# Kernel tuning notes

Hardware: AMD Instinct MI355X
Metric: run time of the kernel (lower is better)

The kernel has to match this reference:

```python
import jax, jax.numpy as jnp
import numpy as np

B, T, D, H = 8192, 2048, 2, 2


def setup_inputs() -> dict:
    key = jax.random.key(0)
    ks = jax.random.split(key, 7)
    return {
        "x": jax.random.normal(ks[0], (B, T, D), dtype=jnp.float32),
        "h0": jax.random.normal(ks[1], (B, H), dtype=jnp.float32),
        "c0": jax.random.normal(ks[2], (B, H), dtype=jnp.float32),
        "w_ih": jax.random.normal(ks[3], (4 * H, D), dtype=jnp.float32),
        "w_hh": jax.random.normal(ks[4], (4 * H, H), dtype=jnp.float32),
        "b_ih": jax.random.normal(ks[5], (4 * H,), dtype=jnp.float32),
        "b_hh": jax.random.normal(ks[6], (4 * H,), dtype=jnp.float32),
    }


def reference(x, h0, c0, w_ih, w_hh, b_ih, b_hh):
    # Precompute input projections for all timesteps in one GEMM: (T, B, 4H)
    xg = jnp.einsum("btd,gd->tbg", x, w_ih) + b_ih

    def step(carry, xt_g):
        h, c = carry
        gates = xt_g + h @ w_hh.T + b_hh  # (B, 4H)
        i, f, g, o = jnp.split(gates, 4, axis=-1)  # torch lstm_cell gate order: i,f,g,o
        c = jax.nn.sigmoid(f) * c + jax.nn.sigmoid(i) * jnp.tanh(g)
        h = jax.nn.sigmoid(o) * jnp.tanh(c)
        return (h, c), None

    (h, c), _ = jax.lax.scan(step, (h0, c0), xg)
    return c
```

## Files before the change

### kernel.cpp

```cpp
#include <hip/hip_runtime.h>


#define LOG2E 1.4426950408889634f

template <int CTRL>
__device__ __forceinline__ float qdpp(float v) {
    int i = __builtin_bit_cast(int, v);
    i = __builtin_amdgcn_update_dpp(0, i, CTRL, 0xf, 0xf, true);
    return __builtin_bit_cast(float, i);
}
#define DPP_HSEL        0x14
#define DPP_BCAST2      0xAA
#define DPP_BCAST3      0xFF
#define DPP_SWAP2       0x4E
#define DPP_HALF_MIRROR 0x141

__global__ __launch_bounds__(64, 1) void lstm_oct_kernel(
    const float* __restrict__ x,
    const float* __restrict__ h0,
    const float* __restrict__ c0,
    const float* __restrict__ w_ih,
    const float* __restrict__ w_hh,
    const float* __restrict__ b_ih,
    const float* __restrict__ b_hh,
    float* __restrict__ out,
    int B, int T)
{
    const int tid = blockIdx.x * blockDim.x + threadIdx.x;
    const int e = tid >> 3;
    const int q = tid & 7;
    if (e >= B) return;

    const int r = (q < 4) ? q : 11 - q;
    const bool isTanh = (q >= 6);
    const bool inQ1   = (q >= 4);
    const bool sel45  = (q == 4) || (q == 5);
    const bool selMid = (q >= 2) && (q <= 5);

    const float a = isTanh ? (2.0f * LOG2E) : (-LOG2E);
    const float m = isTanh ? (-4.0f * LOG2E) : 1.0f;
    const float d = isTanh ? (2.0f * LOG2E) : 0.0f;

    const float wi0 = w_ih[2 * r] * a, wi1 = w_ih[2 * r + 1] * a;
    const float wh0 = w_hh[2 * r] * a, wh1 = w_hh[2 * r + 1] * a;
    const float bias = (b_ih[r] + b_hh[r]) * a;

    const int col = (q & 1) ^ ((q >> 2) & 1);
    float h = h0[2 * e + col];
    float c = c0[2 * e + col] * (2.0f * LOG2E);

    const int NI = T >> 1;
    const float4* __restrict__ xp =
        reinterpret_cast<const float4*>(x) + (size_t)e * NI;

    auto step = [&](float x0, float x1) {
        float hm  = qdpp<DPP_HSEL>(h);
        float hs  = inQ1 ? hm : h;
        float hh0 = qdpp<DPP_BCAST2>(hs);
        float hh1 = qdpp<DPP_BCAST3>(hs);
        float ax = fmaf(wi1, x1, fmaf(wi0, x0, bias));
        float g  = fmaf(wh1, hh1, fmaf(wh0, hh0, ax));
        float n  = fmaf(m, __builtin_amdgcn_rcpf(1.0f + __builtin_amdgcn_exp2f(g)), d);
        float mv = qdpp<DPP_HALF_MIRROR>(n);
        float X = sel45  ? mv : n;
        float Y = selMid ? c  : mv;
        float p = X * Y;
        float ps = qdpp<DPP_SWAP2>(p);
        c = p + ps;
        float tc = fmaf(-2.0f, __builtin_amdgcn_rcpf(1.0f + __builtin_amdgcn_exp2f(c)), 1.0f);
        float Z = sel45 ? n : mv;
        h = Z * tc;
    };

    constexpr int BV = 8;
    float4 A[BV], Bb[BV];

    auto loadbuf = [&](float4* buf, int batch) {
#pragma unroll
        for (int j = 0; j < BV; ++j) buf[j] = xp[batch * BV + j];
    };
    auto consume = [&](const float4* buf) {
#pragma unroll
        for (int j = 0; j < BV; ++j) {
            step(buf[j].x, buf[j].y);
            step(buf[j].z, buf[j].w);
        }
    };

    const int nb = NI / BV;
    int bi = 0;
    if (nb >= 2) {
        loadbuf(A, 0);
        loadbuf(Bb, 1);
        for (bi = 0; bi + 1 < nb; bi += 2) {
            consume(A);
            if (bi + 2 < nb) loadbuf(A, bi + 2);
            consume(Bb);
            if (bi + 3 < nb) loadbuf(Bb, bi + 3);
        }
        if (bi < nb) { consume(A); ++bi; }
    }
    for (int i = bi * BV; i < NI; ++i) {
        float4 v = xp[i];
        step(v.x, v.y);
        step(v.z, v.w);
    }

    if (q < 2) out[2 * e + q] = c * (0.5f / LOG2E);
}

extern "C" void kernel_launch(void* const* d_in, const int* in_sizes, int n_in,
                              void* d_out, int out_size, void* d_ws, size_t ws_size,
                              hipStream_t stream) {
    const float* x    = (const float*)d_in[0];
    const float* h0   = (const float*)d_in[1];
    const float* c0   = (const float*)d_in[2];
    const float* w_ih = (const float*)d_in[3];
    const float* w_hh = (const float*)d_in[4];
    const float* b_ih = (const float*)d_in[5];
    const float* b_hh = (const float*)d_in[6];
    float* out = (float*)d_out;

    const int B = in_sizes[1] / 2;
    const int T = in_sizes[0] / (B * 2);

    const int threads = B * 8;
    dim3 block(64);
    dim3 grid((threads + 63) / 64);
    hipLaunchKernelGGL(lstm_oct_kernel, grid, block, 0, stream,
                       x, h0, c0, w_ih, w_hh, b_ih, b_hh, out, B, T);
}
```

Measured before the change: 323.7 us.

## Fold output gate into recurrent weights and compute tanh(c) from exp products

Restructures the recurrent step so h is never formed explicitly. Each lane keeps tanh(c) and folds the sigmoid(o) factor into per-step effective recurrent weights, taken from neighbouring lanes through masked DPP moves, so the h broadcast and its select drop off the critical dependency chain. tanh(c) is computed from the product of exp2 of the two partial products, letting that exp2 start before the swap-add finishes. In exchange it adds extra DPP moves and multiplies per step, and exp2 of the separate terms can overflow where exp2 of their sum would not, which changes numerics at extreme values.

```diff
diff --git a/kernel.cpp b/kernel.cpp
--- a/kernel.cpp
+++ b/kernel.cpp
@@ -6,16 +6,25 @@
 template <int CTRL>
 __device__ __forceinline__ float qdpp(float v) {
     int i = __builtin_bit_cast(int, v);
-    i = __builtin_amdgcn_update_dpp(0, i, CTRL, 0xf, 0xf, true);
+    i = __builtin_amdgcn_update_dpp(0, i, CTRL, 0xF, 0xF, true);
     return __builtin_bit_cast(float, i);
 }
-#define DPP_HSEL        0x14
-#define DPP_BCAST2      0xAA
-#define DPP_BCAST3      0xFF
-#define DPP_SWAP2       0x4E
-#define DPP_HALF_MIRROR 0x141
+template <int CTRL, int BANK>
+__device__ __forceinline__ float mdpp(float old, float v) {
+    int i = __builtin_amdgcn_update_dpp(__builtin_bit_cast(int, old),
+                                        __builtin_bit_cast(int, v),
+                                        CTRL, 0xF, BANK, false);
+    return __builtin_bit_cast(float, i);
+}
+#define DPP_MIRROR8 0x141
+#define DPP_SWAP2   0x4E
+#define DPP_COLSWP  0xB1
+#define DPP_ZB_OWN0 0xEE
+#define DPP_ZB_OWN1 0x44
+#define DPP_ZB_OTH0 0xBB
+#define DPP_ZB_OTH1 0x11
 
-__global__ __launch_bounds__(64, 1) void lstm_oct_kernel(
+__global__ __launch_bounds__(64, 1) void lstm_oct_nh_kernel(
     const float* __restrict__ x,
     const float* __restrict__ h0,
     const float* __restrict__ c0,
@@ -33,43 +42,50 @@
 
     const int r = (q < 4) ? q : 11 - q;
     const bool isTanh = (q >= 6);
-    const bool inQ1   = (q >= 4);
     const bool sel45  = (q == 4) || (q == 5);
     const bool selMid = (q >= 2) && (q <= 5);
+    const int col = (q & 1) ^ ((q >> 2) & 1);
 
     const float a = isTanh ? (2.0f * LOG2E) : (-LOG2E);
     const float m = isTanh ? (-4.0f * LOG2E) : 1.0f;
     const float d = isTanh ? (2.0f * LOG2E) : 0.0f;
 
-    const float wi0 = w_ih[2 * r] * a, wi1 = w_ih[2 * r + 1] * a;
-    const float wh0 = w_hh[2 * r] * a, wh1 = w_hh[2 * r + 1] * a;
+    const float wx0 = w_ih[2 * r] * a, wx1 = w_ih[2 * r + 1] * a;
     const float bias = (b_ih[r] + b_hh[r]) * a;
+    const float AwhOwn = w_hh[2 * r + col] * a;
+    const float AwhOth = w_hh[2 * r + (1 - col)] * a;
 
-    const int col = (q & 1) ^ ((q >> 2) & 1);
-    float h = h0[2 * e + col];
-    float c = c0[2 * e + col] * (2.0f * LOG2E);
+    float tc = h0[2 * e + col];
+    float cs = c0[2 * e + col] * (2.0f * LOG2E);
+    float WOwn = AwhOwn;
+    float WOth = AwhOth;
 
     const int NI = T >> 1;
     const float4* __restrict__ xp =
         reinterpret_cast<const float4*>(x) + (size_t)e * NI;
 
     auto step = [&](float x0, float x1) {
-        float hm  = qdpp<DPP_HSEL>(h);
-        float hs  = inQ1 ? hm : h;
-        float hh0 = qdpp<DPP_BCAST2>(hs);
-        float hh1 = qdpp<DPP_BCAST3>(hs);
-        float ax = fmaf(wi1, x1, fmaf(wi0, x0, bias));
-        float g  = fmaf(wh1, hh1, fmaf(wh0, hh0, ax));
-        float n  = fmaf(m, __builtin_amdgcn_rcpf(1.0f + __builtin_amdgcn_exp2f(g)), d);
-        float mv = qdpp<DPP_HALF_MIRROR>(n);
-        float X = sel45  ? mv : n;
-        float Y = selMid ? c  : mv;
+        float tco = qdpp<DPP_COLSWP>(tc);
+        float ax  = fmaf(wx1, x1, fmaf(wx0, x0, bias));
+        float g   = fmaf(WOth, tco, fmaf(WOwn, tc, ax));
+        float n   = fmaf(m, __builtin_amdgcn_rcpf(1.0f + __builtin_amdgcn_exp2f(g)), d);
+        float mv  = qdpp<DPP_MIRROR8>(n);
+        float X = sel45 ? mv : n;
+        float Y = selMid ? cs : mv;
         float p = X * Y;
         float ps = qdpp<DPP_SWAP2>(p);
-        c = p + ps;
-        float tc = fmaf(-2.0f, __builtin_amdgcn_rcpf(1.0f + __builtin_amdgcn_exp2f(c)), 1.0f);
+        cs = p + ps;
+        float Ep  = __builtin_amdgcn_exp2f(p);
+        float Eps = qdpp<DPP_SWAP2>(Ep);
+        float r2  = __builtin_amdgcn_rcpf(fmaf(Ep, Eps, 1.0f));
+        tc = fmaf(-2.0f, r2, 1.0f);
         float Z = sel45 ? n : mv;
-        h = Z * tc;
+        float zbOwn = mdpp<DPP_ZB_OWN0, 0x5>(Z, Z);
+        zbOwn = mdpp<DPP_ZB_OWN1, 0xA>(zbOwn, Z);
+        float zbOth = mdpp<DPP_ZB_OTH0, 0x5>(Z, Z);
+        zbOth = mdpp<DPP_ZB_OTH1, 0xA>(zbOth, Z);
+        WOwn = AwhOwn * zbOwn;
+        WOth = AwhOth * zbOth;
     };
 
     constexpr int BV = 8;
@@ -106,7 +122,7 @@
         step(v.z, v.w);
     }
 
-    if (q < 2) out[2 * e + q] = c * (0.5f / LOG2E);
+    if (q < 2) out[2 * e + q] = cs * (0.5f / LOG2E);
 }
 
 extern "C" void kernel_launch(void* const* d_in, const int* in_sizes, int n_in,
@@ -127,6 +143,6 @@
     const int threads = B * 8;
     dim3 block(64);
     dim3 grid((threads + 63) / 64);
-    hipLaunchKernelGGL(lstm_oct_kernel, grid, block, 0, stream,
+    hipLaunchKernelGGL(lstm_oct_nh_kernel, grid, block, 0, stream,
                        x, h0, c0, w_ih, w_hh, b_ih, b_hh, out, B, T);
 }
```

Measured after the change: 322.2 us. About the same (-0.5%).
